# Kernel tuning notes

Measured on AMD Instinct MI355X. Metric: run time of the kernel, lower is better.

The kernel has to match this reference:

```python
import jax, jax.numpy as jnp
import numpy as np

N = 50000        # nodes
E = 500000       # edges
NUM = 4          # sampled intermediate neighbors per edge (self.num)
F = 64           # in_feats == out_feats (transform=False)
D = 32           # dist_dim
NB = 64          # embedding rows = len(boundaries)+1


def setup_inputs() -> dict:
    key = jax.random.key(0)
    ks = jax.random.split(key, 10)
    feat = jax.random.normal(ks[0], (N, F), jnp.float32)
    loc = jax.random.uniform(ks[1], (N, 3), jnp.float32)          # 3D positions in unit cube
    boundaries = jnp.sort(jax.random.uniform(ks[2], (NB - 1,), jnp.float32, 0.0, 2.0))
    embed_table = jax.random.normal(ks[3], (NB, D), jnp.float32)
    G_w = jax.random.normal(ks[4], (F, D), jnp.float32) / np.sqrt(D)      # Linear(dist_dim->out, no bias)
    agg_w = jax.random.normal(ks[5], (F, 2 * F), jnp.float32) / np.sqrt(2 * F)  # Linear(2*out->out)
    agg_b = jnp.zeros((F,), jnp.float32)
    src = jax.random.randint(ks[6], (E,), 0, N, jnp.int32)
    dst = jax.random.randint(ks[7], (E,), 0, N, jnp.int32)
    inter_ids = jax.random.randint(ks[8], (E, NUM), 0, N, jnp.int32)
    return dict(feat=feat, loc=loc, boundaries=boundaries, embed_table=embed_table,
                G_w=G_w, agg_w=agg_w, agg_b=agg_b, src=src, dst=dst, inter_ids=inter_ids)


def reference(feat, loc, boundaries, embed_table, G_w, agg_w, agg_b, src, dst, inter_ids):
    n = feat.shape[0]
    ones = jnp.ones((src.shape[0],), feat.dtype)
    # symmetric-ish degree normalization: d0 = in_deg^-0.5, d2 = out_deg^-0.5
    in_deg = jax.ops.segment_sum(ones, dst, num_segments=n)
    out_deg = jax.ops.segment_sum(ones, src, num_segments=n)
    d0 = jnp.clip(in_deg, 1.0) ** -0.5   # [N]
    d2 = jnp.clip(out_deg, 1.0) ** -0.5  # [N]

    # dist1 = ||loc[dst] - loc[src]||_2, bucketize -> embed -> G
    dist1 = jnp.linalg.norm(loc[dst] - loc[src], axis=1)              # [E]
    de1 = embed_table[jnp.searchsorted(boundaries, dist1)] @ G_w.T    # [E, F]

    # intermediate sampled neighbors: dist to each sampled node from edge src
    pos_src = loc[src]                                                # [E, 3]
    inter_pos = loc[inter_ids]                                        # [E, NUM, 3]
    dist_ = jnp.linalg.norm(pos_src[:, None, :] - inter_pos, axis=-1) # [E, NUM]
    de_ = embed_table[jnp.searchsorted(boundaries, dist_)] @ G_w.T    # [E, NUM, F]
    inter_h = feat[inter_ids]                                         # [E, NUM, F]
    dist_embed_dot_h = (de_ * inter_h).mean(axis=1)                   # [E, F]

    # h = d0[dst] * d2[src] * agg_fc([de1 * h_src, dist_embed_dot_h])
    cat = jnp.concatenate([de1 * feat[src], dist_embed_dot_h], axis=1)  # [E, 2F]
    msg = (d0[dst] * d2[src])[:, None] * (cat @ agg_w.T + agg_b)        # [E, F]

    # update_all(copy_e('h'), sum) -> scatter-sum messages to dst
    ft = jax.ops.segment_sum(msg, dst, num_segments=n)                  # [N, F]
    return ft
```

## Files before the change

### kernel.cpp

```cpp
#include <hip/hip_runtime.h>
#include <math.h>

#define LUTN 1024
#define LUTSCALE 512.0f


__global__ __launch_bounds__(256) void prep_kernel(
    const float* __restrict__ embed, const float* __restrict__ G_w,
    const float* __restrict__ boundaries, const float* __restrict__ feat,
    const float* __restrict__ loc,
    float* __restrict__ M, int* __restrict__ lut,
    int* __restrict__ d2i, int* __restrict__ cnt,
    unsigned short* __restrict__ featH, float4* __restrict__ loc4, int N) {

    const int gid = blockIdx.x * 256 + threadIdx.x;
    const int gsz = gridDim.x * 256;
    for (int i = gid; i < N; i += gsz) { cnt[i] = 0; d2i[i] = 0; }
    for (int i = gid; i < 4096; i += gsz) {
        int b = i >> 6, f = i & 63;
        float acc = 0.f;
        #pragma unroll
        for (int dd = 0; dd < 32; ++dd) acc += embed[b * 32 + dd] * G_w[f * 32 + dd];
        M[i] = acc;
    }
    for (int i = gid; i < LUTN; i += gsz) {
        float left = (float)i * (1.0f / LUTSCALE);
        int c = 0;
        for (int j = 0; j < 63; ++j) c += (boundaries[j] < left) ? 1 : 0;
        lut[i] = c;
    }
    const int nq = N * 16;
    for (int i = gid; i < nq; i += gsz) {
        float4 v = ((const float4*)feat)[i];
        unsigned ux = __float_as_uint(v.x), uy = __float_as_uint(v.y);
        unsigned uz = __float_as_uint(v.z), uw = __float_as_uint(v.w);
        ushort4 h;
        h.x = (unsigned short)((ux + 0x7FFFu + ((ux >> 16) & 1u)) >> 16);
        h.y = (unsigned short)((uy + 0x7FFFu + ((uy >> 16) & 1u)) >> 16);
        h.z = (unsigned short)((uz + 0x7FFFu + ((uz >> 16) & 1u)) >> 16);
        h.w = (unsigned short)((uw + 0x7FFFu + ((uw >> 16) & 1u)) >> 16);
        ((ushort4*)featH)[i] = h;
    }
    for (int i = gid; i < N; i += gsz)
        loc4[i] = make_float4(loc[3 * i], loc[3 * i + 1], loc[3 * i + 2], 0.f);
}


__global__ __launch_bounds__(256) void edge_kernel(
    const float4* __restrict__ loc4, const float* __restrict__ boundaries,
    const int* __restrict__ lut,
    const int* __restrict__ src, const int* __restrict__ dst,
    const int* __restrict__ inter,
    int* __restrict__ cnt, int* __restrict__ d2i,
    int4* __restrict__ recE, int E) {

    __shared__ int lut_s[LUTN];
    __shared__ float bl[64];
    ((int4*)lut_s)[threadIdx.x] = ((const int4*)lut)[threadIdx.x];
    if (threadIdx.x < 64)
        bl[threadIdx.x] = (threadIdx.x < 63) ? boundaries[threadIdx.x] : 3.4e38f;
    __syncthreads();

    const int e = blockIdx.x * 256 + threadIdx.x;
    if (e >= E) return;

    const int s = src[e], d = dst[e];
    const int4 ii = ((const int4*)inter)[e];

    const float4 ps = loc4[s];
    float dist[5];
    {
        float4 pd = loc4[d];
        float dx = pd.x - ps.x, dy = pd.y - ps.y, dz = pd.z - ps.z;
        dist[0] = sqrtf(dx * dx + dy * dy + dz * dz);
    }
    const int id4[4] = {ii.x, ii.y, ii.z, ii.w};
    #pragma unroll
    for (int j = 0; j < 4; ++j) {
        float4 pt = loc4[id4[j]];
        float dx = pt.x - ps.x, dy = pt.y - ps.y, dz = pt.z - ps.z;
        dist[1 + j] = sqrtf(dx * dx + dy * dy + dz * dz);
    }
    unsigned pack = 0;
    #pragma unroll
    for (int q = 0; q < 5; ++q) {
        float dq = dist[q];
        int cell = (int)(dq * LUTSCALE);
        cell = (cell > LUTN - 1) ? (LUTN - 1) : cell;
        int b = lut_s[cell];
        while (b < 63 && bl[b] < dq) ++b;
        while (b > 0 && bl[b - 1] >= dq) --b;
        pack |= ((unsigned)b) << (6 * q);
    }

    const int r = atomicAdd(&cnt[d], 1);
    atomicAdd(&d2i[s], 1);

    recE[e] = make_int4(s | (ii.x << 16), ii.y | (ii.z << 16), ii.w | (r << 16), (int)pack);
}


__global__ __launch_bounds__(1024) void scan_block_kernel(
    const int* __restrict__ cnt, int* __restrict__ startv,
    int* __restrict__ part, int N) {

    __shared__ int wsum[16];
    const int t = threadIdx.x, lane = t & 63, wv = t >> 6;
    const int i = blockIdx.x * 1024 + t;

    int v = (i < N) ? cnt[i] : 0;
    int x = v;
    #pragma unroll
    for (int off = 1; off < 64; off <<= 1) { int y = __shfl_up(x, off); if (lane >= off) x += y; }
    if (lane == 63) wsum[wv] = x;
    __syncthreads();
    if (t < 16) {
        int w = wsum[t], xx = w;
        #pragma unroll
        for (int off = 1; off < 16; off <<= 1) { int y = __shfl_up(xx, off); if (t >= off) xx += y; }
        wsum[t] = xx - w;
    }
    __syncthreads();
    int incl = x + wsum[wv];
    if (i < N) startv[i] = incl - v;
    if (t == 1023) part[blockIdx.x] = incl;
}

__device__ __forceinline__ void load_chunkoff(const int* __restrict__ part, int nb,
                                              int* __restrict__ co) {
    if (threadIdx.x < 64) {
        int v = (threadIdx.x < nb) ? part[threadIdx.x] : 0;
        int x = v;
        #pragma unroll
        for (int off = 1; off < 64; off <<= 1) {
            int y = __shfl_up(x, off);
            if ((threadIdx.x & 63) >= off) x += y;
        }
        co[threadIdx.x] = x - v;
    }
    __syncthreads();
}


__global__ __launch_bounds__(256) void scatter_kernel(
    const int4* __restrict__ recE, const int* __restrict__ dst,
    const int* __restrict__ startv, const int* __restrict__ part,
    const int* __restrict__ d2i, int4* __restrict__ rec, int E, int nb) {

    __shared__ int co[64];
    load_chunkoff(part, nb, co);

    const int e = blockIdx.x * 256 + threadIdx.x;
    if (e >= E) return;
    const int4 a = recE[e];
    const int s = a.x & 0xFFFF;
    const int r = ((unsigned)a.z) >> 16;
    const int d = dst[e];
    const int pos = startv[d] + co[d >> 10] + r;
    const float w = rsqrtf(fmaxf((float)d2i[s], 1.0f));
    unsigned uw = __float_as_uint(w);
    unsigned wb = (uw + 0x7FFFu + ((uw >> 16) & 1u)) & 0xFFFF0000u;
    rec[pos] = make_int4(a.x, a.y, (a.z & 0xFFFF) | (int)wb, a.w);
}


__global__ __launch_bounds__(256) void node_kernel(
    const unsigned short* __restrict__ featH, const float* __restrict__ M,
    const int* __restrict__ cnt, const int* __restrict__ startv,
    const int* __restrict__ part, const int4* __restrict__ rec,
    float* __restrict__ cat, float* __restrict__ swb, int N, int nb) {

    __shared__ float Ms[4096];
    __shared__ int co[64];
    #pragma unroll
    for (int i = 0; i < 4; ++i)
        ((float4*)Ms)[threadIdx.x + 256 * i] = ((const float4*)M)[threadIdx.x + 256 * i];
    load_chunkoff(part, nb, co);

    const int lane = threadIdx.x & 63;
    const int wid  = threadIdx.x >> 6;
    const int d    = blockIdx.x * 4 + wid;
    if (d >= N) return;

    const int deg  = __builtin_amdgcn_readfirstlane(cnt[d]);
    const int base = __builtin_amdgcn_readfirstlane(startv[d] + co[d >> 10]);
    const int4* rp = rec + base;

    float acc0 = 0.f, acc1 = 0.f, sw = 0.f;

    #pragma unroll 4
    for (int k = 0; k < deg; ++k) {
        const int4 r = rp[k];
        const int s  = r.x & 0xFFFF;
        const int i0 = ((unsigned)r.x) >> 16;
        const int i1 = r.y & 0xFFFF;
        const int i2 = ((unsigned)r.y) >> 16;
        const int i3 = r.z & 0xFFFF;
        const float w = __uint_as_float((unsigned)r.z & 0xFFFF0000u);
        const unsigned pk = (unsigned)r.w;

        const float fs = __uint_as_float(((unsigned)featH[(size_t)s  * 64 + lane]) << 16);
        const float f0 = __uint_as_float(((unsigned)featH[(size_t)i0 * 64 + lane]) << 16);
        const float f1 = __uint_as_float(((unsigned)featH[(size_t)i1 * 64 + lane]) << 16);
        const float f2 = __uint_as_float(((unsigned)featH[(size_t)i2 * 64 + lane]) << 16);
        const float f3 = __uint_as_float(((unsigned)featH[(size_t)i3 * 64 + lane]) << 16);
        const float m0 = Ms[(pk & 63u) * 64 + lane];
        const float m1 = Ms[((pk >> 6) & 63u) * 64 + lane];
        const float m2 = Ms[((pk >> 12) & 63u) * 64 + lane];
        const float m3 = Ms[((pk >> 18) & 63u) * 64 + lane];
        const float m4 = Ms[((pk >> 24) & 63u) * 64 + lane];

        acc0 = fmaf(m0 * fs, w, acc0);
        float t = m1 * f0 + m2 * f1 + m3 * f2 + m4 * f3;
        acc1 = fmaf(0.25f * t, w, acc1);
        sw += w;
    }

    cat[(size_t)d * 128 + lane]      = acc0;
    cat[(size_t)d * 128 + 64 + lane] = acc1;
    if (lane == 0) swb[d] = sw;
}


__global__ __launch_bounds__(256) void epilogue_kernel(
    const float* __restrict__ cat, const float* __restrict__ agg_w,
    const float* __restrict__ agg_b, const float* __restrict__ swb,
    const int* __restrict__ cnt, float* __restrict__ out, int N) {

    const int lane = threadIdx.x & 63;
    const int wid  = threadIdx.x >> 6;

    float4 aw[32];
    const float4* awp = (const float4*)(agg_w + (size_t)lane * 128);
    #pragma unroll
    for (int i = 0; i < 32; ++i) aw[i] = awp[i];
    const float bias = agg_b[lane];

    const int gw = blockIdx.x * 4 + wid;
    const int stride = gridDim.x * 4;

    for (int d0i = gw; d0i < N; d0i += stride) {
        const int du = __builtin_amdgcn_readfirstlane(d0i);
        const float* cp = cat + (size_t)du * 128;
        float a0 = bias * swb[du], a1 = 0.f, a2 = 0.f, a3 = 0.f;
        #pragma unroll
        for (int k4 = 0; k4 < 32; k4 += 4) {
            float4 c0 = ((const float4*)cp)[k4];
            float4 c1 = ((const float4*)cp)[k4 + 1];
            float4 c2 = ((const float4*)cp)[k4 + 2];
            float4 c3 = ((const float4*)cp)[k4 + 3];
            a0 = fmaf(aw[k4].x, c0.x, a0); a0 = fmaf(aw[k4].y, c0.y, a0);
            a0 = fmaf(aw[k4].z, c0.z, a0); a0 = fmaf(aw[k4].w, c0.w, a0);
            a1 = fmaf(aw[k4+1].x, c1.x, a1); a1 = fmaf(aw[k4+1].y, c1.y, a1);
            a1 = fmaf(aw[k4+1].z, c1.z, a1); a1 = fmaf(aw[k4+1].w, c1.w, a1);
            a2 = fmaf(aw[k4+2].x, c2.x, a2); a2 = fmaf(aw[k4+2].y, c2.y, a2);
            a2 = fmaf(aw[k4+2].z, c2.z, a2); a2 = fmaf(aw[k4+2].w, c2.w, a2);
            a3 = fmaf(aw[k4+3].x, c3.x, a3); a3 = fmaf(aw[k4+3].y, c3.y, a3);
            a3 = fmaf(aw[k4+3].z, c3.z, a3); a3 = fmaf(aw[k4+3].w, c3.w, a3);
        }
        const float d0v = rsqrtf(fmaxf((float)cnt[du], 1.0f));
        out[(size_t)du * 64 + lane] = d0v * ((a0 + a1) + (a2 + a3));
    }
}


extern "C" void kernel_launch(void* const* d_in, const int* in_sizes, int n_in,
                              void* d_out, int out_size, void* d_ws, size_t ws_size,
                              hipStream_t stream) {
    const float* feat       = (const float*)d_in[0];
    const float* loc        = (const float*)d_in[1];
    const float* boundaries = (const float*)d_in[2];
    const float* embed      = (const float*)d_in[3];
    const float* G_w        = (const float*)d_in[4];
    const float* agg_w      = (const float*)d_in[5];
    const float* agg_b      = (const float*)d_in[6];
    const int*   src        = (const int*)d_in[7];
    const int*   dst        = (const int*)d_in[8];
    const int*   inter      = (const int*)d_in[9];

    const int N = in_sizes[0] / 64;
    const int E = in_sizes[7];

    char* w = (char*)d_ws;
    auto take = [&](size_t bytes) { char* p = w; w += (bytes + 15) & ~(size_t)15; return p; };
    float*          M      = (float*)take(4096 * 4);
    int*            lut    = (int*)  take(LUTN * 4);
    int*            d2i    = (int*)  take((size_t)N * 4);
    int*            cnt    = (int*)  take((size_t)N * 4);
    int*            startv = (int*)  take((size_t)N * 4);
    int*            part   = (int*)  take(64 * 4);
    int4*           recE   = (int4*) take((size_t)E * 16);
    int4*           rec    = (int4*) take((size_t)E * 16);
    float*          cat    = (float*)take((size_t)N * 128 * 4);
    float*          swb    = (float*)take((size_t)N * 4);
    unsigned short* featH  = (unsigned short*)take((size_t)N * 64 * 2);
    float4*         loc4   = (float4*)take((size_t)N * 16);
    float*          out    = (float*)d_out;

    const int eb = (E + 255) / 256;
    const int nb = (N + 1023) / 1024;

    prep_kernel<<<1024, 256, 0, stream>>>(embed, G_w, boundaries, feat, loc,
                                          M, lut, d2i, cnt, featH, loc4, N);
    edge_kernel<<<eb, 256, 0, stream>>>(loc4, boundaries, lut, src, dst, inter,
                                        cnt, d2i, recE, E);
    scan_block_kernel<<<nb, 1024, 0, stream>>>(cnt, startv, part, N);
    scatter_kernel<<<eb, 256, 0, stream>>>(recE, dst, startv, part, d2i, rec, E, nb);
    node_kernel<<<(N + 3) / 4, 256, 0, stream>>>(featH, M, cnt, startv, part, rec,
                                                 cat, swb, N, nb);
    epilogue_kernel<<<768, 256, 0, stream>>>(cat, agg_w, agg_b, swb, cnt, out, N);
}
```

Baseline: 229.4 us.

## Split edge work into role-specialized blocks and overlap histogram, bucketing, bf16 conversion

The edge kernel becomes a single launch whose blocks take different roles: some do the degree and rank atomics over pairs of edges, some compute distances and buckets for two edges per thread, and the rest convert features to bf16. Feature conversion and counter zeroing move out of the prep kernel, with zeroing done by a memset. Ranks are stored in a separate ushort array instead of being packed into the record. The aim is to overlap latency-bound atomic work with the gather-heavy bucketing and bandwidth-bound conversion, at the cost of an extra rank array and an extra memset launch.

```diff
diff --git a/kernel.cpp b/kernel.cpp
--- a/kernel.cpp
+++ b/kernel.cpp
@@ -5,17 +5,14 @@
 #define LUTSCALE 512.0f
 
 
-__global__ __launch_bounds__(256) void prep_kernel(
+__global__ __launch_bounds__(256) void prep0_kernel(
     const float* __restrict__ embed, const float* __restrict__ G_w,
-    const float* __restrict__ boundaries, const float* __restrict__ feat,
-    const float* __restrict__ loc,
+    const float* __restrict__ boundaries, const float* __restrict__ loc,
     float* __restrict__ M, int* __restrict__ lut,
-    int* __restrict__ d2i, int* __restrict__ cnt,
-    unsigned short* __restrict__ featH, float4* __restrict__ loc4, int N) {
+    float4* __restrict__ loc4, int N) {
 
     const int gid = blockIdx.x * 256 + threadIdx.x;
     const int gsz = gridDim.x * 256;
-    for (int i = gid; i < N; i += gsz) { cnt[i] = 0; d2i[i] = 0; }
     for (int i = gid; i < 4096; i += gsz) {
         int b = i >> 6, f = i & 63;
         float acc = 0.f;
@@ -29,30 +26,62 @@
         for (int j = 0; j < 63; ++j) c += (boundaries[j] < left) ? 1 : 0;
         lut[i] = c;
     }
-    const int nq = N * 16;
-    for (int i = gid; i < nq; i += gsz) {
-        float4 v = ((const float4*)feat)[i];
-        unsigned ux = __float_as_uint(v.x), uy = __float_as_uint(v.y);
-        unsigned uz = __float_as_uint(v.z), uw = __float_as_uint(v.w);
-        ushort4 h;
-        h.x = (unsigned short)((ux + 0x7FFFu + ((ux >> 16) & 1u)) >> 16);
-        h.y = (unsigned short)((uy + 0x7FFFu + ((uy >> 16) & 1u)) >> 16);
-        h.z = (unsigned short)((uz + 0x7FFFu + ((uz >> 16) & 1u)) >> 16);
-        h.w = (unsigned short)((uw + 0x7FFFu + ((uw >> 16) & 1u)) >> 16);
-        ((ushort4*)featH)[i] = h;
-    }
     for (int i = gid; i < N; i += gsz)
         loc4[i] = make_float4(loc[3 * i], loc[3 * i + 1], loc[3 * i + 2], 0.f);
 }
 
 
-__global__ __launch_bounds__(256) void edge_kernel(
+__global__ __launch_bounds__(256) void main_kernel(
     const float4* __restrict__ loc4, const float* __restrict__ boundaries,
-    const int* __restrict__ lut,
+    const int* __restrict__ lut, const float* __restrict__ feat,
     const int* __restrict__ src, const int* __restrict__ dst,
     const int* __restrict__ inter,
     int* __restrict__ cnt, int* __restrict__ d2i,
-    int4* __restrict__ recE, int E) {
+    unsigned short* __restrict__ rnk, int4* __restrict__ recE,
+    unsigned short* __restrict__ featH,
+    int N, int E, int HB, int GB, int FB) {
+
+    if (blockIdx.x < HB) {
+        const int t = blockIdx.x * 256 + threadIdx.x;
+        const int nth = HB * 256;
+        const int nq = E >> 1;
+        for (int q = t; q < nq; q += nth) {
+            const int2 s2 = ((const int2*)src)[q];
+            const int2 d2 = ((const int2*)dst)[q];
+            int r0 = atomicAdd(&cnt[d2.x], 1);
+            int r1 = atomicAdd(&cnt[d2.y], 1);
+            atomicAdd(&d2i[s2.x], 1);
+            atomicAdd(&d2i[s2.y], 1);
+            ushort2 rr;
+            rr.x = (unsigned short)r0;
+            rr.y = (unsigned short)r1;
+            ((ushort2*)rnk)[q] = rr;
+        }
+        for (int e = (nq << 1) + t; e < E; e += nth) {
+            int r = atomicAdd(&cnt[dst[e]], 1);
+            atomicAdd(&d2i[src[e]], 1);
+            rnk[e] = (unsigned short)r;
+        }
+        return;
+    }
+
+    if (blockIdx.x >= HB + GB) {
+        const int t = (blockIdx.x - HB - GB) * 256 + threadIdx.x;
+        const int nth = FB * 256;
+        const int nq = N * 16;
+        for (int i = t; i < nq; i += nth) {
+            float4 v = ((const float4*)feat)[i];
+            unsigned ux = __float_as_uint(v.x), uy = __float_as_uint(v.y);
+            unsigned uz = __float_as_uint(v.z), uw = __float_as_uint(v.w);
+            ushort4 h;
+            h.x = (unsigned short)((ux + 0x7FFFu + ((ux >> 16) & 1u)) >> 16);
+            h.y = (unsigned short)((uy + 0x7FFFu + ((uy >> 16) & 1u)) >> 16);
+            h.z = (unsigned short)((uz + 0x7FFFu + ((uz >> 16) & 1u)) >> 16);
+            h.w = (unsigned short)((uw + 0x7FFFu + ((uw >> 16) & 1u)) >> 16);
+            ((ushort4*)featH)[i] = h;
+        }
+        return;
+    }
 
     __shared__ int lut_s[LUTN];
     __shared__ float bl[64];
@@ -61,42 +90,42 @@
         bl[threadIdx.x] = (threadIdx.x < 63) ? boundaries[threadIdx.x] : 3.4e38f;
     __syncthreads();
 
-    const int e = blockIdx.x * 256 + threadIdx.x;
-    if (e >= E) return;
-
-    const int s = src[e], d = dst[e];
-    const int4 ii = ((const int4*)inter)[e];
-
-    const float4 ps = loc4[s];
-    float dist[5];
-    {
-        float4 pd = loc4[d];
-        float dx = pd.x - ps.x, dy = pd.y - ps.y, dz = pd.z - ps.z;
-        dist[0] = sqrtf(dx * dx + dy * dy + dz * dz);
-    }
-    const int id4[4] = {ii.x, ii.y, ii.z, ii.w};
+    const int base = (blockIdx.x - HB) * 512 + threadIdx.x;
     #pragma unroll
-    for (int j = 0; j < 4; ++j) {
-        float4 pt = loc4[id4[j]];
-        float dx = pt.x - ps.x, dy = pt.y - ps.y, dz = pt.z - ps.z;
-        dist[1 + j] = sqrtf(dx * dx + dy * dy + dz * dz);
-    }
-    unsigned pack = 0;
-    #pragma unroll
-    for (int q = 0; q < 5; ++q) {
-        float dq = dist[q];
-        int cell = (int)(dq * LUTSCALE);
-        cell = (cell > LUTN - 1) ? (LUTN - 1) : cell;
-        int b = lut_s[cell];
-        while (b < 63 && bl[b] < dq) ++b;
-        while (b > 0 && bl[b - 1] >= dq) --b;
-        pack |= ((unsigned)b) << (6 * q);
-    }
-
-    const int r = atomicAdd(&cnt[d], 1);
-    atomicAdd(&d2i[s], 1);
-
-    recE[e] = make_int4(s | (ii.x << 16), ii.y | (ii.z << 16), ii.w | (r << 16), (int)pack);
+    for (int u = 0; u < 2; ++u) {
+        const int e = base + u * 256;
+        if (e >= E) continue;
+
+        const int s = src[e], d = dst[e];
+        const int4 ii = ((const int4*)inter)[e];
+
+        const float4 ps = loc4[s];
+        float dist[5];
+        {
+            float4 pd = loc4[d];
+            float dx = pd.x - ps.x, dy = pd.y - ps.y, dz = pd.z - ps.z;
+            dist[0] = sqrtf(dx * dx + dy * dy + dz * dz);
+        }
+        const int id4[4] = {ii.x, ii.y, ii.z, ii.w};
+        #pragma unroll
+        for (int j = 0; j < 4; ++j) {
+            float4 pt = loc4[id4[j]];
+            float dx = pt.x - ps.x, dy = pt.y - ps.y, dz = pt.z - ps.z;
+            dist[1 + j] = sqrtf(dx * dx + dy * dy + dz * dz);
+        }
+        unsigned pack = 0;
+        #pragma unroll
+        for (int q = 0; q < 5; ++q) {
+            float dq = dist[q];
+            int cell = (int)(dq * LUTSCALE);
+            cell = (cell > LUTN - 1) ? (LUTN - 1) : cell;
+            int b = lut_s[cell];
+            while (b < 63 && bl[b] < dq) ++b;
+            while (b > 0 && bl[b - 1] >= dq) --b;
+            pack |= ((unsigned)b) << (6 * q);
+        }
+        recE[e] = make_int4(s | (ii.x << 16), ii.y | (ii.z << 16), ii.w, (int)pack);
+    }
 }
 
 
@@ -144,6 +173,7 @@
 
 __global__ __launch_bounds__(256) void scatter_kernel(
     const int4* __restrict__ recE, const int* __restrict__ dst,
+    const unsigned short* __restrict__ rnk,
     const int* __restrict__ startv, const int* __restrict__ part,
     const int* __restrict__ d2i, int4* __restrict__ rec, int E, int nb) {
 
@@ -154,7 +184,7 @@
     if (e >= E) return;
     const int4 a = recE[e];
     const int s = a.x & 0xFFFF;
-    const int r = ((unsigned)a.z) >> 16;
+    const int r = rnk[e];
     const int d = dst[e];
     const int pos = startv[d] + co[d >> 10] + r;
     const float w = rsqrtf(fmaxf((float)d2i[s], 1.0f));
@@ -285,12 +315,13 @@
     auto take = [&](size_t bytes) { char* p = w; w += (bytes + 15) & ~(size_t)15; return p; };
     float*          M      = (float*)take(4096 * 4);
     int*            lut    = (int*)  take(LUTN * 4);
-    int*            d2i    = (int*)  take((size_t)N * 4);
-    int*            cnt    = (int*)  take((size_t)N * 4);
+    int*            d2i    = (int*)  take((size_t)2 * N * 4);
+    int*            cnt    = d2i + N;
     int*            startv = (int*)  take((size_t)N * 4);
     int*            part   = (int*)  take(64 * 4);
     int4*           recE   = (int4*) take((size_t)E * 16);
     int4*           rec    = (int4*) take((size_t)E * 16);
+    unsigned short* rnk    = (unsigned short*)take((size_t)E * 2);
     float*          cat    = (float*)take((size_t)N * 128 * 4);
     float*          swb    = (float*)take((size_t)N * 4);
     unsigned short* featH  = (unsigned short*)take((size_t)N * 64 * 2);
@@ -300,12 +331,18 @@
     const int eb = (E + 255) / 256;
     const int nb = (N + 1023) / 1024;
 
-    prep_kernel<<<1024, 256, 0, stream>>>(embed, G_w, boundaries, feat, loc,
-                                          M, lut, d2i, cnt, featH, loc4, N);
-    edge_kernel<<<eb, 256, 0, stream>>>(loc4, boundaries, lut, src, dst, inter,
-                                        cnt, d2i, recE, E);
+    const int HB = (E / 2 + 255) / 256;
+    const int GB = (E + 511) / 512;
+    const int FB = 512;
+
+    hipMemsetAsync(d2i, 0, (size_t)2 * N * sizeof(int), stream);
+    prep0_kernel<<<256, 256, 0, stream>>>(embed, G_w, boundaries, loc, M, lut, loc4, N);
+    main_kernel<<<HB + GB + FB, 256, 0, stream>>>(loc4, boundaries, lut, feat,
+                                                  src, dst, inter,
+                                                  cnt, d2i, rnk, recE, featH,
+                                                  N, E, HB, GB, FB);
     scan_block_kernel<<<nb, 1024, 0, stream>>>(cnt, startv, part, N);
-    scatter_kernel<<<eb, 256, 0, stream>>>(recE, dst, startv, part, d2i, rec, E, nb);
+    scatter_kernel<<<eb, 256, 0, stream>>>(recE, dst, rnk, startv, part, d2i, rec, E, nb);
     node_kernel<<<(N + 3) / 4, 256, 0, stream>>>(featH, M, cnt, startv, part, rec,
                                                  cat, swb, N, nb);
     epilogue_kernel<<<768, 256, 0, stream>>>(cat, agg_w, agg_b, swb, cnt, out, N);
```

Result: slower. 249.6 us (+8.8%).

## Replace global atomic degree counting with per-chunk shared-memory byte histograms

Applied to the files above, without the earlier changes.

Global atomics on cnt and d2i in the edge kernel are replaced by a histogram kernel. Each block counts in-degree and out-degree for a 2048-edge chunk in shared memory, with four 8-bit counters packed per word, and records each edge's rank within its chunk. A merge kernel prefix-sums the per-chunk counts per node to produce total degrees and per-chunk offsets, and computes the rsqrt source weight. Scatter then builds the position from chunk offset plus local rank. This removes contended global atomics but adds two kernels and streams about 245 chunks × 50K bytes twice through the merge, with strided column reads.

```diff
diff --git a/kernel.cpp b/kernel.cpp
--- a/kernel.cpp
+++ b/kernel.cpp
@@ -3,6 +3,8 @@
 
 #define LUTN 1024
 #define LUTSCALE 512.0f
+#define NBINS 50048
+#define CHSH 11
 
 
 __global__ __launch_bounds__(256) void prep_kernel(
@@ -10,12 +12,10 @@
     const float* __restrict__ boundaries, const float* __restrict__ feat,
     const float* __restrict__ loc,
     float* __restrict__ M, int* __restrict__ lut,
-    int* __restrict__ d2i, int* __restrict__ cnt,
     unsigned short* __restrict__ featH, float4* __restrict__ loc4, int N) {
 
     const int gid = blockIdx.x * 256 + threadIdx.x;
     const int gsz = gridDim.x * 256;
-    for (int i = gid; i < N; i += gsz) { cnt[i] = 0; d2i[i] = 0; }
     for (int i = gid; i < 4096; i += gsz) {
         int b = i >> 6, f = i & 63;
         float acc = 0.f;
@@ -46,12 +46,40 @@
 }
 
 
+__global__ __launch_bounds__(256) void hist_kernel(
+    const int* __restrict__ src, const int* __restrict__ dst,
+    unsigned char* __restrict__ pcnt, unsigned char* __restrict__ psrc,
+    unsigned char* __restrict__ rnk8, int E) {
+
+    __shared__ unsigned int hc[NBINS / 4];
+    __shared__ unsigned int hs[NBINS / 4];
+    for (int i = threadIdx.x; i < NBINS / 4; i += 256) { hc[i] = 0u; hs[i] = 0u; }
+    __syncthreads();
+
+    const int base = blockIdx.x << CHSH;
+    const int lim  = min(E - base, 1 << CHSH);
+    for (int t = threadIdx.x; t < lim; t += 256) {
+        const int e = base + t;
+        const int d = dst[e];
+        const int s = src[e];
+        const unsigned sh = (unsigned)(d & 3) * 8u;
+        unsigned old = atomicAdd(&hc[d >> 2], 1u << sh);
+        rnk8[e] = (unsigned char)((old >> sh) & 0xFFu);
+        atomicAdd(&hs[s >> 2], 1u << ((unsigned)(s & 3) * 8u));
+    }
+    __syncthreads();
+
+    unsigned int* gc = (unsigned int*)(pcnt + (size_t)blockIdx.x * NBINS);
+    unsigned int* gs = (unsigned int*)(psrc + (size_t)blockIdx.x * NBINS);
+    for (int i = threadIdx.x; i < NBINS / 4; i += 256) { gc[i] = hc[i]; gs[i] = hs[i]; }
+}
+
+
 __global__ __launch_bounds__(256) void edge_kernel(
     const float4* __restrict__ loc4, const float* __restrict__ boundaries,
     const int* __restrict__ lut,
     const int* __restrict__ src, const int* __restrict__ dst,
     const int* __restrict__ inter,
-    int* __restrict__ cnt, int* __restrict__ d2i,
     int4* __restrict__ recE, int E) {
 
     __shared__ int lut_s[LUTN];
@@ -92,11 +120,31 @@
         while (b > 0 && bl[b - 1] >= dq) --b;
         pack |= ((unsigned)b) << (6 * q);
     }
-
-    const int r = atomicAdd(&cnt[d], 1);
-    atomicAdd(&d2i[s], 1);
-
-    recE[e] = make_int4(s | (ii.x << 16), ii.y | (ii.z << 16), ii.w | (r << 16), (int)pack);
+    recE[e] = make_int4(s | (ii.x << 16), ii.y | (ii.z << 16), ii.w, (int)pack);
+}
+
+
+__global__ __launch_bounds__(256) void merge_kernel(
+    unsigned char* __restrict__ pcnt, const unsigned char* __restrict__ psrc,
+    int* __restrict__ cnt, float* __restrict__ d2w, int P, int N) {
+
+    const int d = blockIdx.x * 256 + threadIdx.x;
+    if (d >= N) return;
+
+    int sc = 0;
+    #pragma unroll 4
+    for (int p = 0; p < P; ++p) {
+        const size_t idx = (size_t)p * NBINS + d;
+        const int c = pcnt[idx];
+        pcnt[idx] = (unsigned char)sc;
+        sc += c;
+    }
+    cnt[d] = sc;
+
+    int ss = 0;
+    #pragma unroll 4
+    for (int p = 0; p < P; ++p) ss += psrc[(size_t)p * NBINS + d];
+    d2w[d] = rsqrtf(fmaxf((float)ss, 1.0f));
 }
 
 
@@ -144,8 +192,10 @@
 
 __global__ __launch_bounds__(256) void scatter_kernel(
     const int4* __restrict__ recE, const int* __restrict__ dst,
+    const unsigned char* __restrict__ rnk8,
     const int* __restrict__ startv, const int* __restrict__ part,
-    const int* __restrict__ d2i, int4* __restrict__ rec, int E, int nb) {
+    const unsigned char* __restrict__ pcnt, const float* __restrict__ d2w,
+    int4* __restrict__ rec, int E, int nb) {
 
     __shared__ int co[64];
     load_chunkoff(part, nb, co);
@@ -154,10 +204,11 @@
     if (e >= E) return;
     const int4 a = recE[e];
     const int s = a.x & 0xFFFF;
-    const int r = ((unsigned)a.z) >> 16;
     const int d = dst[e];
-    const int pos = startv[d] + co[d >> 10] + r;
-    const float w = rsqrtf(fmaxf((float)d2i[s], 1.0f));
+    const int p = e >> CHSH;
+    const int base = pcnt[(size_t)p * NBINS + d];
+    const int pos = startv[d] + co[d >> 10] + base + (int)rnk8[e];
+    const float w = d2w[s];
     unsigned uw = __float_as_uint(w);
     unsigned wb = (uw + 0x7FFFu + ((uw >> 16) & 1u)) & 0xFFFF0000u;
     rec[pos] = make_int4(a.x, a.y, (a.z & 0xFFFF) | (int)wb, a.w);
@@ -281,16 +332,21 @@
     const int N = in_sizes[0] / 64;
     const int E = in_sizes[7];
 
+    const int P = (E + (1 << CHSH) - 1) >> CHSH;
+
     char* w = (char*)d_ws;
     auto take = [&](size_t bytes) { char* p = w; w += (bytes + 15) & ~(size_t)15; return p; };
     float*          M      = (float*)take(4096 * 4);
     int*            lut    = (int*)  take(LUTN * 4);
-    int*            d2i    = (int*)  take((size_t)N * 4);
     int*            cnt    = (int*)  take((size_t)N * 4);
     int*            startv = (int*)  take((size_t)N * 4);
     int*            part   = (int*)  take(64 * 4);
+    float*          d2w    = (float*)take((size_t)N * 4);
     int4*           recE   = (int4*) take((size_t)E * 16);
     int4*           rec    = (int4*) take((size_t)E * 16);
+    unsigned char*  rnk8   = (unsigned char*)take((size_t)E);
+    unsigned char*  pcnt   = (unsigned char*)take((size_t)P * NBINS);
+    unsigned char*  psrc   = (unsigned char*)take((size_t)P * NBINS);
     float*          cat    = (float*)take((size_t)N * 128 * 4);
     float*          swb    = (float*)take((size_t)N * 4);
     unsigned short* featH  = (unsigned short*)take((size_t)N * 64 * 2);
@@ -299,13 +355,16 @@
 
     const int eb = (E + 255) / 256;
     const int nb = (N + 1023) / 1024;
+    const int mb = (N + 255) / 256;
 
     prep_kernel<<<1024, 256, 0, stream>>>(embed, G_w, boundaries, feat, loc,
-                                          M, lut, d2i, cnt, featH, loc4, N);
-    edge_kernel<<<eb, 256, 0, stream>>>(loc4, boundaries, lut, src, dst, inter,
-                                        cnt, d2i, recE, E);
+                                          M, lut, featH, loc4, N);
+    hist_kernel<<<P, 256, 0, stream>>>(src, dst, pcnt, psrc, rnk8, E);
+    edge_kernel<<<eb, 256, 0, stream>>>(loc4, boundaries, lut, src, dst, inter, recE, E);
+    merge_kernel<<<mb, 256, 0, stream>>>(pcnt, psrc, cnt, d2w, P, N);
     scan_block_kernel<<<nb, 1024, 0, stream>>>(cnt, startv, part, N);
-    scatter_kernel<<<eb, 256, 0, stream>>>(recE, dst, startv, part, d2i, rec, E, nb);
+    scatter_kernel<<<eb, 256, 0, stream>>>(recE, dst, rnk8, startv, part, pcnt, d2w,
+                                           rec, E, nb);
     node_kernel<<<(N + 3) / 4, 256, 0, stream>>>(featH, M, cnt, startv, part, rec,
                                                  cat, swb, N, nb);
     epilogue_kernel<<<768, 256, 0, stream>>>(cat, agg_w, agg_b, swb, cnt, out, N);
```

Measured after the change: 254.5 us. 10.9% more time.
